# Kernel tuning notes

Measured on AMD Instinct MI355X. Metric: run time of the kernel, lower is better.

Reference implementation:

```python
import jax, jax.numpy as jnp
import numpy as np

D = 2048      # d_model
H = 16        # n_heads
DH = 128      # head dim
ROPE = 64     # qk_rope_dim = dh//2
NOPE = 64     # qk_nope_dim = dh//2
QP = 1024     # q_proj_dim = int(D*0.5)
KVP = 1365    # kv_proj_dim = int(D*2/3)
THETA = 10000.0
B, S = 2, 2048


def _ln(x, w, b):
    m = x.mean(-1, keepdims=True)
    v = ((x - m) ** 2).mean(-1, keepdims=True)
    return (x - m) / jnp.sqrt(v + 1e-5) * w + b


def _rot_half(x):
    x1, x2 = jnp.split(x, 2, axis=-1)
    return jnp.concatenate([-x2, x1], axis=-1)


def _rope_tables(seq_len):
    # freqs over full dh (as in torch buffer), then slice first ROPE//2 and repeat(...,2)
    freqs = 1.0 / (THETA ** (jnp.arange(0, DH, 2, dtype=jnp.float32) / DH))  # (DH//2,)
    emb = jnp.arange(seq_len, dtype=jnp.float32)[:, None] * freqs[None, :]   # (S, DH//2)
    c = jnp.cos(emb)[:, : ROPE // 2]
    s = jnp.sin(emb)[:, : ROPE // 2]
    cos = jnp.concatenate([c, c], axis=-1)  # (S, ROPE)  matches .repeat(1,1,1,2)
    sin = jnp.concatenate([s, s], axis=-1)
    return cos, sin


def setup_inputs() -> dict:
    ks = jax.random.split(jax.random.key(0), 8)
    p = lambda i, shape: 0.01 * jax.random.normal(ks[i], shape, dtype=jnp.float32)
    return {
        "query": jax.random.normal(ks[0], (B, S, D), dtype=jnp.float32),
        "W_dq": p(1, (D, QP)),
        "W_uq": p(2, (QP, D)),
        "q_ln_w": jnp.ones((QP,), jnp.float32),
        "q_ln_b": jnp.zeros((QP,), jnp.float32),
        "W_dkv": p(3, (D, KVP + ROPE)),
        "W_ukv": p(4, (KVP, D + H * NOPE)),
        "kv_ln_w": jnp.ones((KVP,), jnp.float32),
        "kv_ln_b": jnp.zeros((KVP,), jnp.float32),
        "W_o": p(5, (D, D)),
    }


def reference(query, W_dq, W_uq, q_ln_w, q_ln_b, W_dkv, W_ukv, kv_ln_w, kv_ln_b, W_o):
    b, sq, _ = query.shape
    # Q low-rank path
    cq = _ln(query @ W_dq, q_ln_w, q_ln_b)                       # (B,S,QP)
    Q = (cq @ W_uq).reshape(b, sq, H, DH).transpose(0, 2, 1, 3)  # (B,H,S,DH)
    Qn, Qr = Q[..., :NOPE], Q[..., NOPE:]
    cos, sin = _rope_tables(sq)                                  # (S,ROPE)
    Qr = Qr * cos + _rot_half(Qr) * sin
    # KV low-rank path
    compressed_kv = query @ W_dkv                                # (B,S,KVP+ROPE)
    kv_lat, Kr = compressed_kv[..., :KVP], compressed_kv[..., KVP:]
    kv_lat = _ln(kv_lat, kv_ln_w, kv_ln_b)
    KV = (kv_lat @ W_ukv).reshape(b, sq, H, DH + NOPE).transpose(0, 2, 1, 3)
    Kn, V = KV[..., :NOPE], KV[..., NOPE:]                       # (B,H,S,NOPE),(B,H,S,DH)
    Kr = Kr * cos + _rot_half(Kr) * sin                          # (B,S,ROPE) shared head
    qh = jnp.concatenate([Qn, Qr], axis=-1)                      # (B,H,S,DH)
    kh = jnp.concatenate([Kn, jnp.broadcast_to(Kr[:, None], (b, H, sq, ROPE))], axis=-1)
    # causal attention, scale 1/sqrt(dh) as in SDPA
    scores = jnp.einsum('bhqd,bhkd->bhqk', qh, kh) / jnp.sqrt(jnp.float32(DH))
    mask = jnp.tril(jnp.ones((sq, sq), dtype=bool))
    scores = jnp.where(mask, scores, -jnp.inf)
    attn = jax.nn.softmax(scores, axis=-1)
    out = jnp.einsum('bhqk,bhkd->bhqd', attn, V).transpose(0, 2, 1, 3).reshape(b, sq, D)
    output = out @ W_o.T                                          # nn.Linear, no bias
    return output, compressed_kv
```

## Files before the change

### kernel.cpp

```cpp
#include <hip/hip_runtime.h>

#define BB_   2
#define S_    2048
#define D_    2048
#define H_    16
#define DH_   128
#define ROPE_ 64
#define QP_   1024
#define KVP_  1365
#define KVPR_ 1429
#define KVP_PAD_ 1408
#define NKV_PAD_ 1536
#define NCOMB_ 2560
#define MT_   4096
#define UKV_N_ 3072

typedef unsigned short u16;
typedef unsigned int   u32;
typedef __attribute__((ext_vector_type(4))) u16    u16x4;
typedef __attribute__((ext_vector_type(8))) u16    u16x8;
typedef __attribute__((ext_vector_type(4))) u32    u32x4;
typedef __attribute__((ext_vector_type(8))) __bf16 bf16x8;
typedef __attribute__((ext_vector_type(4))) float  f32x4;
typedef __attribute__((ext_vector_type(16))) float f32x16;

#define NEG_BIG (-1.0e30f)
#define F32_FLAG_BITS 0x49742400u

__device__ __forceinline__ float bf2f(u16 u) {
    u32 x = ((u32)u) << 16;
    return __builtin_bit_cast(float, x);
}
__device__ __forceinline__ u16 f2bf(float f) {
    u32 u = __builtin_bit_cast(u32, f);
    u32 r = u + 0x7fffu + ((u >> 16) & 1u);
    return (u16)(r >> 16);
}
__device__ __forceinline__ u32 pk2(float a, float b) {
    __bf16 x = (__bf16)a, y = (__bf16)b;
    return (u32)__builtin_bit_cast(u16, x) | ((u32)__builtin_bit_cast(u16, y) << 16);
}
__device__ __forceinline__ bf16x8 ld_bf8(const u16* p) {
    u16x8 v = *(const u16x8*)p;
    return __builtin_bit_cast(bf16x8, v);
}
__device__ __forceinline__ bool flag_f32(const u32* flag) { return flag[0] > F32_FLAG_BITS; }

__device__ __forceinline__ void async16(const void* g, void* l) {
    __builtin_amdgcn_global_load_lds(
        (const __attribute__((address_space(1))) void*)g,
        (__attribute__((address_space(3))) void*)l, 16, 0, 0);
}

__global__ __launch_bounds__(256) void detect_kernel(const u16* __restrict__ q, u32* __restrict__ flag)
{
    u32 m = 0;
    for (int i = blockIdx.x * 256 + threadIdx.x; i < (1 << 20); i += 64 * 256) {
        float v = fabsf(bf2f(q[i]));
        u32 b = __builtin_bit_cast(u32, v);
        m = m > b ? m : b;
    }
    #pragma unroll
    for (int off = 32; off; off >>= 1) {
        u32 o = (u32)__shfl_xor((int)m, off, 64);
        m = m > o ? m : o;
    }
    if ((threadIdx.x & 63) == 0) atomicMax(flag, m);
}

__global__ __launch_bounds__(256) void cast_merged_kernel(
    const void* __restrict__ qin, const void* __restrict__ woin,
    u16* __restrict__ q_bf, u16* __restrict__ wo_bf, const u32* __restrict__ flag)
{
    bool f32 = flag_f32(flag);
    const void* in; u16* out; long n;
    if (blockIdx.z == 0) { in = qin;  out = q_bf;  n = (long)MT_ * D_; }
    else                 { in = woin; out = wo_bf; n = (long)D_ * D_; if (blockIdx.x >= 2048) return; }
    long i0 = ((long)blockIdx.x * 256 + threadIdx.x) * 8;
    if (i0 >= n) return;
    u16x8 o;
    if (f32) {
        const float* p = (const float*)in + i0;
        #pragma unroll
        for (int j = 0; j < 8; j++) o[j] = f2bf(p[j]);
    } else {
        o = *(const u16x8*)((const u16*)in + i0);
    }
    *(u16x8*)(out + i0) = o;
}

template <int MODE>
__global__ __launch_bounds__(256) void gemm_bt(
    const u16* __restrict__ A, const u16* __restrict__ Bt,
    void* __restrict__ Cout, int M, int N, int K,
    const float* __restrict__ cosT, const float* __restrict__ sinT,
    u16* __restrict__ khp, const u32* __restrict__ flag)
{
    __shared__ u16 As[2][128 * 32];
    __shared__ u16 Bs[2][128 * 32];
    const int tid  = threadIdx.x;
    const int lane = tid & 63;
    const int wave = tid >> 6;
    const int m0 = blockIdx.x * 128;
    const int n0 = blockIdx.y * 128;
    const int wr = (wave >> 1) * 64;
    const int wc = (wave & 1) * 64;
    const bool f32o = (MODE == 2) ? flag_f32(flag) : false;

    const int srow = lane >> 2;
    const int scol = (lane & 3) * 8;
    const u16* aptr0 = A  + (long)(m0 + wave * 32 + srow) * K + scol;
    const u16* bptr0 = Bt + (long)(n0 + wave * 32 + srow) * K + scol;
    const int woff = (wave * 32) * 32;

    f32x4 acc[4][4] = {};

    const int row16 = lane & 15;
    const int kq = (lane >> 4) * 8;

    auto stage = [&](int buf, int kt) {
        u16* asl = &As[buf][woff];
        u16* bsl = &Bs[buf][woff];
        async16(aptr0 + kt,          asl);
        async16(aptr0 + 16 * K + kt, asl + 16 * 32);
        async16(bptr0 + kt,          bsl);
        async16(bptr0 + 16 * K + kt, bsl + 16 * 32);
    };
    auto compute = [&](int buf) {
        bf16x8 a[4], b[4];
        #pragma unroll
        for (int i = 0; i < 4; i++)
            a[i] = ld_bf8(&As[buf][(wr + i * 16 + row16) * 32 + kq]);
        #pragma unroll
        for (int j = 0; j < 4; j++)
            b[j] = ld_bf8(&Bs[buf][(wc + j * 16 + row16) * 32 + kq]);
        #pragma unroll
        for (int i = 0; i < 4; i++)
            #pragma unroll
            for (int j = 0; j < 4; j++)
                acc[i][j] = __builtin_amdgcn_mfma_f32_16x16x32_bf16(a[i], b[j], acc[i][j], 0, 0, 0);
    };

    stage(0, 0);
    __syncthreads();
    const int nk = K >> 5;
    for (int t = 0; t < nk; t += 2) {
        stage(1, (t + 1) * 32);
        compute(0);
        __syncthreads();
        if (t + 2 < nk) stage(0, (t + 2) * 32);
        compute(1);
        __syncthreads();
    }

    const int crow = wr + (lane >> 4) * 4;
    const int ccol = wc + row16;

    if (MODE == 3) {
        const int h = (int)blockIdx.y;
        u16* qhp = (u16*)Cout;
        #pragma unroll
        for (int i = 0; i < 4; i++) {
            #pragma unroll
            for (int r = 0; r < 4; r++) {
                int row = m0 + crow + i * 16 + r;
                int b = row >> 11, s = row & 2047;
                long obase = (((long)(b * 16 + h)) * 2048 + s) * 128;
                if (wc == 0) {
                    #pragma unroll
                    for (int j = 0; j < 4; j++)
                        qhp[obase + j * 16 + row16] = f2bf(acc[i][j][r]);
                } else {
                    float c0 = cosT[s * 32 + row16],      s0 = sinT[s * 32 + row16];
                    float c1 = cosT[s * 32 + 16 + row16], s1 = sinT[s * 32 + 16 + row16];
                    float x0 = acc[i][0][r], x1 = acc[i][1][r];
                    float x2 = acc[i][2][r], x3 = acc[i][3][r];
                    qhp[obase + 64 + row16]  = f2bf(x0 * c0 - x2 * s0);
                    qhp[obase + 80 + row16]  = f2bf(x1 * c1 - x3 * s1);
                    qhp[obase + 96 + row16]  = f2bf(x2 * c0 + x0 * s0);
                    qhp[obase + 112 + row16] = f2bf(x3 * c1 + x1 * s1);
                }
            }
        }
        return;
    }
    if (MODE == 4) {
        #pragma unroll
        for (int i = 0; i < 4; i++) {
            #pragma unroll
            for (int r = 0; r < 4; r++) {
                int row = m0 + crow + i * 16 + r;
                int b = row >> 11, s = row & 2047;
                #pragma unroll
                for (int j = 0; j < 4; j++) {
                    int c = n0 + wc + j * 16 + row16;
                    int h = c / 192, dd = c - h * 192;
                    u16 v16 = f2bf(acc[i][j][r]);
                    if (dd < 64)
                        khp[(((long)(b * 16 + h)) * 2048 + s) * 128 + dd] = v16;
                    else
                        ((u16*)Cout)[(long)row * N + c] = v16;
                }
            }
        }
        return;
    }

    #pragma unroll
    for (int i = 0; i < 4; i++) {
        #pragma unroll
        for (int r = 0; r < 4; r++) {
            long row = m0 + crow + i * 16 + r;
            #pragma unroll
            for (int j = 0; j < 4; j++) {
                float v = acc[i][j][r];
                long col = n0 + ccol + j * 16;
                if (MODE == 2 && f32o) ((float*)Cout)[row * N + col] = v;
                else                   ((u16*)Cout)[row * N + col] = f2bf(v);
            }
        }
    }
}

__global__ __launch_bounds__(256) void transpose_all_kernel(
    const void* __restrict__ w_dq, const void* __restrict__ w_dkv,
    const void* __restrict__ w_uq, const void* __restrict__ w_ukv,
    u16* __restrict__ wcomb, u16* __restrict__ wuqT, u16* __restrict__ wukvT,
    const u32* __restrict__ flag)
{
    const void* in; u16* out; int Rin, Cin, Nout, Kpad, gx, gy;
    switch (blockIdx.z) {
        case 0: in = w_dq;  out = wcomb;                       Rin = 2048; Cin = 1024;   Nout = 1024;     Kpad = 2048;     gx = 64; gy = 32; break;
        case 1: in = w_dkv; out = wcomb + (size_t)1024 * 2048; Rin = 2048; Cin = KVPR_;  Nout = NKV_PAD_; Kpad = 2048;     gx = 64; gy = 48; break;
        case 2: in = w_uq;  out = wuqT;                        Rin = 1024; Cin = 2048;   Nout = 2048;     Kpad = 1024;     gx = 32; gy = 64; break;
        default:in = w_ukv; out = wukvT;                       Rin = KVP_; Cin = UKV_N_; Nout = UKV_N_;   Kpad = KVP_PAD_; gx = 44; gy = 96; break;
    }
    if ((int)blockIdx.x >= gx || (int)blockIdx.y >= gy) return;
    __shared__ u16 t[32][33];
    bool f32 = flag_f32(flag);
    int k0 = blockIdx.x * 32, n0 = blockIdx.y * 32;
    int tx = threadIdx.x & 31, ty = threadIdx.x >> 5;
    #pragma unroll
    for (int rr = 0; rr < 4; ++rr) {
        int k = k0 + ty + rr * 8, n = n0 + tx;
        u16 v = 0;
        if (k < Rin && n < Cin)
            v = f32 ? f2bf(((const float*)in)[(long)k * Cin + n])
                    : ((const u16*)in)[(long)k * Cin + n];
        t[ty + rr * 8][tx] = v;
    }
    __syncthreads();
    #pragma unroll
    for (int rr = 0; rr < 4; ++rr) {
        int n = n0 + ty + rr * 8, k = k0 + tx;
        if (n < Nout && k < Kpad) out[(long)n * Kpad + k] = t[tx][ty + rr * 8];
    }
}

__device__ __forceinline__ float block_sum(float v, float* red) {
    #pragma unroll
    for (int off = 32; off; off >>= 1) v += __shfl_xor(v, off, 64);
    int wv = threadIdx.x >> 6;
    __syncthreads();
    if ((threadIdx.x & 63) == 0) red[wv] = v;
    __syncthreads();
    return red[0] + red[1] + red[2] + red[3];
}

__global__ __launch_bounds__(256) void ln_both_kernel(
    const u16* __restrict__ x, const void* __restrict__ qw, const void* __restrict__ qb,
    const void* __restrict__ kw, const void* __restrict__ kb,
    u16* __restrict__ cq, u16* __restrict__ kv_lat, void* __restrict__ d_out,
    u16* __restrict__ kh, const float* __restrict__ cosT, const float* __restrict__ sinT,
    const u32* __restrict__ flag)
{
    __shared__ float red[4];
    __shared__ float kr[64];
    bool f32 = flag_f32(flag);
    long row = blockIdx.x;
    const int tid = threadIdx.x;

    if (blockIdx.z == 0) {
        const u16* xr = x + row * NCOMB_;
        float v[4]; float s = 0.f;
        #pragma unroll
        for (int i = 0; i < 4; i++) { v[i] = bf2f(xr[tid + i * 256]); s += v[i]; }
        float mean = block_sum(s, red) * (1.0f / QP_);
        float var = 0.f;
        #pragma unroll
        for (int i = 0; i < 4; i++) { float d = v[i] - mean; var += d * d; }
        var = block_sum(var, red) * (1.0f / QP_);
        float rstd = rsqrtf(var + 1e-5f);
        #pragma unroll
        for (int i = 0; i < 4; i++) {
            int idx = tid + i * 256;
            float wv = f32 ? ((const float*)qw)[idx] : bf2f(((const u16*)qw)[idx]);
            float bv = f32 ? ((const float*)qb)[idx] : bf2f(((const u16*)qb)[idx]);
            cq[row * QP_ + idx] = f2bf((v[i] - mean) * rstd * wv + bv);
        }
    } else {
        const int b = (int)(row >> 11), s_ = (int)(row & 2047);
        const u16* xr = x + row * NCOMB_ + QP_;
        u16 u[6]; float v[6]; float s = 0.f;
        #pragma unroll
        for (int i = 0; i < 6; i++) {
            int idx = tid + i * 256;
            u[i] = xr[idx];
            v[i] = bf2f(u[i]);
            if (idx >= KVP_ && idx < KVPR_) kr[idx - KVP_] = v[i];
            if (idx < KVP_) s += v[i];
        }
        float mean = block_sum(s, red) * (1.0f / KVP_);
        float var = 0.f;
        #pragma unroll
        for (int i = 0; i < 6; i++) {
            int idx = tid + i * 256;
            if (idx < KVP_) { float d = v[i] - mean; var += d * d; }
        }
        var = block_sum(var, red) * (1.0f / KVP_);
        float rstd = rsqrtf(var + 1e-5f);

        float* out1f = (float*)d_out + (size_t)MT_ * D_;
        u16*   out1h = (u16*)d_out   + (size_t)MT_ * D_;
        #pragma unroll
        for (int i = 0; i < 6; i++) {
            int idx = tid + i * 256;
            if (idx < KVPR_) {
                if (f32) out1f[row * KVPR_ + idx] = v[i];
                else     out1h[row * KVPR_ + idx] = u[i];
            }
            if (idx < KVP_PAD_) {
                float wv = 0.f, bv = 0.f;
                if (idx < KVP_) {
                    wv = f32 ? ((const float*)kw)[idx] : bf2f(((const u16*)kw)[idx]);
                    bv = f32 ? ((const float*)kb)[idx] : bf2f(((const u16*)kb)[idx]);
                }
                u16 o = 0;
                if (idx < KVP_) o = f2bf((v[i] - mean) * rstd * wv + bv);
                kv_lat[row * KVP_PAD_ + idx] = o;
            }
            if (idx >= KVP_ && idx < KVPR_) {
                int r = idx - KVP_;
                float xr_ = kr[r];
                float xo = (r < 32) ? -kr[r + 32] : kr[r - 32];
                int m = r & 31;
                u16 vv = f2bf(xr_ * cosT[s_ * 32 + m] + xo * sinT[s_ * 32 + m]);
                #pragma unroll
                for (int h = 0; h < 16; h++)
                    kh[(((long)(b * 16 + h)) * 2048 + s_) * 128 + 64 + r] = vv;
            }
        }
    }
}

__global__ void rope_tab_kernel(float* __restrict__ cosT, float* __restrict__ sinT, u32* __restrict__ flag) {
    int idx = blockIdx.x * 256 + threadIdx.x;
    if (idx == 0) flag[0] = 0u;
    if (idx >= S_ * 32) return;
    int pos = idx >> 5, i = idx & 31;
    float freq = (float)exp(-((double)i / 64.0) * log(10000.0));
    float ang = (float)pos * freq;
    cosT[idx] = (float)cos((double)ang);
    sinT[idx] = (float)sin((double)ang);
}

__global__ __launch_bounds__(256) void pack_vt_kernel(const u16* __restrict__ KV, u16* __restrict__ Vt)
{
    int bh = blockIdx.x; int b = bh >> 4, h = bh & 15;
    int s0 = blockIdx.y * 64;
    __shared__ u16 t[64][136];
    #pragma unroll
    for (int it = 0; it < 4; ++it) {
        int ch = threadIdx.x + it * 256;
        int sr = ch >> 4, c8 = (ch & 15) * 8;
        *(u16x8*)&t[sr][c8] = *(const u16x8*)&KV[((long)(b * S_ + s0 + sr)) * 3072 + h * 192 + 64 + c8];
    }
    __syncthreads();
    #pragma unroll
    for (int it = 0; it < 4; ++it) {
        int ch = threadIdx.x + it * 256;
        int d = ch >> 3, s8 = (ch & 7) * 8;
        u16x8 v;
        #pragma unroll
        for (int j = 0; j < 8; j++) v[j] = t[s8 + j][d];
        *(u16x8*)&Vt[((long)bh * 128 + d) * S_ + s0 + s8] = v;
    }
}

#define ATT_SCALE 0.08838834764831845f
#define K_LOG2E (ATT_SCALE * 1.4426950408889634f)
#define DEFER_THR 62.0f

__global__ __launch_bounds__(256, 2) void attn_kernel(
    const u16* __restrict__ qh, const u16* __restrict__ kh,
    const u16* __restrict__ Vt, u16* __restrict__ attn_out)
{
    __shared__ u16 Ks[64 * 128];
    __shared__ u16 Vs[128 * 64];

    const int bh = (int)blockIdx.x + ((int)blockIdx.z << 3);
    const int b = bh >> 4, h = bh & 15;
    const int jq = ((int)blockIdx.z < 2) ? (15 - (int)blockIdx.y) : (int)blockIdx.y;
    const int qbase = jq * 128;
    const int tid = threadIdx.x;
    const int lane = tid & 63;
    const int w = tid >> 6;
    const int l5 = lane & 31;
    const int hi = lane >> 5;
    const int wq0 = qbase + w * 32;
    const int qg = wq0 + l5;
    const int kend = qbase + 128;
    const int kend_w = wq0 + 32;

    bf16x8 qb[8];
    {
        const u16* qp = &qh[((long)bh * S_ + qg) * 128 + 8 * hi];
        #pragma unroll
        for (int kc = 0; kc < 8; kc++)
            qb[kc] = ld_bf8(qp + kc * 16);
    }

    f32x16 o[4] = {};
    float m_run = NEG_BIG;
    float l_run = 0.f;

    const long khb = (long)bh * S_;

    u16x8 kst[4], vst[4];
    auto load_kv = [&](int k0) {
        #pragma unroll
        for (int it = 0; it < 4; ++it) {
            int r = w * 16 + it * 4 + (lane >> 4);
            kst[it] = *(const u16x8*)&kh[(khb + k0 + r) * 128 + (((lane & 15) ^ (r & 7)) << 3)];
        }
        #pragma unroll
        for (int it = 0; it < 4; ++it) {
            int d = w * 32 + it * 8 + (lane >> 3);
            vst[it] = *(const u16x8*)&Vt[((long)bh * 128 + d) * S_ + k0 + (((lane & 7) ^ (d & 7)) << 3)];
        }
    };

    load_kv(0);

    for (int k0 = 0; k0 < kend; k0 += 64) {
        __syncthreads();
        #pragma unroll
        for (int it = 0; it < 4; ++it)
            *(u16x8*)&Ks[(w * 16 + it * 4) * 128 + lane * 8] = kst[it];
        #pragma unroll
        for (int it = 0; it < 4; ++it)
            *(u16x8*)&Vs[(w * 32 + it * 8) * 64 + lane * 8] = vst[it];
        __syncthreads();
        if (k0 + 64 < kend) load_kv(k0 + 64);

        if (k0 < kend_w) {
            f32x16 sc[2] = {};
            #pragma unroll
            for (int kc = 0; kc < 8; kc++) {
                #pragma unroll
                for (int ct = 0; ct < 2; ct++) {
                    int krow = ct * 32 + l5;
                    bf16x8 kf = ld_bf8(&Ks[krow * 128 + (((2 * kc + hi) ^ (krow & 7)) << 3)]);
                    sc[ct] = __builtin_amdgcn_mfma_f32_32x32x16_bf16(kf, qb[kc], sc[ct], 0, 0, 0);
                }
            }
            if (k0 + 64 > wq0) {
                #pragma unroll
                for (int ct = 0; ct < 2; ct++)
                    #pragma unroll
                    for (int g = 0; g < 4; g++)
                        #pragma unroll
                        for (int t = 0; t < 4; t++)
                            sc[ct][g * 4 + t] =
                                (k0 + ct * 32 + g * 8 + t + 4 * hi <= qg) ? sc[ct][g * 4 + t] : NEG_BIG;
            }
            float m = sc[0][0];
            #pragma unroll
            for (int i = 1; i < 16; i++) m = fmaxf(m, sc[0][i]);
            #pragma unroll
            for (int i = 0; i < 16; i++) m = fmaxf(m, sc[1][i]);
            m = fmaxf(m, __shfl_xor(m, 32, 64));
            bool ok = (m <= m_run + DEFER_THR);
            if (!__all((int)ok)) {
                float mn = fmaxf(m_run, m);
                float alpha = exp2f((m_run - mn) * K_LOG2E);
                m_run = mn;
                l_run *= alpha;
                #pragma unroll
                for (int dt = 0; dt < 4; dt++)
                    #pragma unroll
                    for (int i = 0; i < 16; i++) o[dt][i] *= alpha;
            }
            float mk = m_run * K_LOG2E;
            float s = 0.f;
            #pragma unroll
            for (int ct = 0; ct < 2; ct++)
                #pragma unroll
                for (int i = 0; i < 16; i++) {
                    float p = exp2f(fmaf(sc[ct][i], K_LOG2E, -mk));
                    sc[ct][i] = p;
                    s += p;
                }
            l_run += s + __shfl_xor(s, 32, 64);
            bf16x8 pb[4];
            #pragma unroll
            for (int ct = 0; ct < 2; ct++)
                #pragma unroll
                for (int c2 = 0; c2 < 2; c2++) {
                    u32 lo0 = pk2(sc[ct][8 * c2 + 0], sc[ct][8 * c2 + 1]);
                    u32 lo1 = pk2(sc[ct][8 * c2 + 2], sc[ct][8 * c2 + 3]);
                    u32 h0  = pk2(sc[ct][8 * c2 + 4], sc[ct][8 * c2 + 5]);
                    u32 h1  = pk2(sc[ct][8 * c2 + 6], sc[ct][8 * c2 + 7]);
                    u32 s0 = hi ? lo0 : h0;
                    u32 s1 = hi ? lo1 : h1;
                    u32 r0 = (u32)__shfl_xor((int)s0, 32, 64);
                    u32 r1 = (u32)__shfl_xor((int)s1, 32, 64);
                    u32x4 f;
                    f[0] = hi ? r0 : lo0;
                    f[1] = hi ? r1 : lo1;
                    f[2] = hi ? h0 : r0;
                    f[3] = hi ? h1 : r1;
                    pb[ct * 2 + c2] = __builtin_bit_cast(bf16x8, f);
                }
            #pragma unroll
            for (int kk = 0; kk < 4; kk++) {
                #pragma unroll
                for (int dt = 0; dt < 4; dt++) {
                    int drow = dt * 32 + l5;
                    bf16x8 vf = ld_bf8(&Vs[drow * 64 + (((2 * kk + hi) ^ (drow & 7)) << 3)]);
                    o[dt] = __builtin_amdgcn_mfma_f32_32x32x16_bf16(vf, pb[kk], o[dt], 0, 0, 0);
                }
            }
        }
    }

    float inv = 1.0f / l_run;
    const long orow = ((long)b * S_ + qg) * 2048 + h * 128;
    #pragma unroll
    for (int dt = 0; dt < 4; dt++)
        #pragma unroll
        for (int g = 0; g < 4; g++) {
            u16x4 v;
            #pragma unroll
            for (int t = 0; t < 4; t++) v[t] = f2bf(o[dt][g * 4 + t] * inv);
            *(u16x4*)&attn_out[orow + dt * 32 + g * 8 + 4 * hi] = v;
        }
}

#define MIB(x) ((size_t)(x) << 20)
extern "C" void kernel_launch(void* const* d_in, const int* in_sizes, int n_in,
                              void* d_out, int out_size, void* d_ws, size_t ws_size,
                              hipStream_t stream)
{
    const void* query  = d_in[0];
    const void* W_dq   = d_in[1];
    const void* W_uq   = d_in[2];
    const void* q_ln_w = d_in[3];
    const void* q_ln_b = d_in[4];
    const void* W_dkv  = d_in[5];
    const void* W_ukv  = d_in[6];
    const void* kv_ln_w = d_in[7];
    const void* kv_ln_b = d_in[8];
    const void* W_o    = d_in[9];
    (void)ws_size; (void)in_sizes; (void)n_in; (void)out_size;

    char* base = (char*)d_ws;
    u32*   flag     = (u32*)base;
    float* rope_cos = (float*)(base + 4096);
    float* rope_sin = (float*)(base + 266240);
    u16* qh     = (u16*)(base + MIB(1));
    u16* kh     = (u16*)(base + MIB(17));
    u16* Vt     = (u16*)(base + MIB(33));
    u16* q_bf   = (u16*)(base + MIB(49));
    u16* Wo_bf  = (u16*)(base + MIB(65));
    u16* Wcomb  = (u16*)(base + MIB(73));
    u16* cqkv   = (u16*)(base + MIB(83));
    u16* cq     = (u16*)(base + MIB(103));
    u16* kv_lat = (u16*)(base + MIB(111));
    u16* WuqT   = (u16*)(base + MIB(122));
    u16* WukvT  = (u16*)(base + MIB(126));
    u16* KV     = (u16*)(base + MIB(73));
    u16* attn_o = (u16*)(base + MIB(73));

    rope_tab_kernel<<<(S_ * 32 + 255) / 256, 256, 0, stream>>>(rope_cos, rope_sin, flag);
    detect_kernel<<<64, 256, 0, stream>>>((const u16*)query, flag);

    cast_merged_kernel<<<dim3(4096, 1, 2), 256, 0, stream>>>(query, W_o, q_bf, Wo_bf, flag);
    transpose_all_kernel<<<dim3(64, 96, 4), 256, 0, stream>>>(W_dq, W_dkv, W_uq, W_ukv,
                                                              Wcomb, WuqT, WukvT, flag);

    gemm_bt<0><<<dim3(32, 20), 256, 0, stream>>>(q_bf, Wcomb, cqkv, MT_, NCOMB_, D_,
                                                 nullptr, nullptr, nullptr, flag);
    ln_both_kernel<<<dim3(MT_, 1, 2), 256, 0, stream>>>(cqkv, q_ln_w, q_ln_b, kv_ln_w, kv_ln_b,
                                                        cq, kv_lat, d_out, kh,
                                                        rope_cos, rope_sin, flag);

    gemm_bt<3><<<dim3(32, 16), 256, 0, stream>>>(cq, WuqT, qh, MT_, D_, QP_,
                                                 rope_cos, rope_sin, nullptr, flag);

    gemm_bt<4><<<dim3(32, 24), 256, 0, stream>>>(kv_lat, WukvT, KV, MT_, UKV_N_, KVP_PAD_,
                                                 nullptr, nullptr, kh, flag);
    pack_vt_kernel<<<dim3(32, 32), 256, 0, stream>>>(KV, Vt);

    attn_kernel<<<dim3(8, 16, 4), 256, 0, stream>>>(qh, kh, Vt, attn_o);
    gemm_bt<2><<<dim3(32, 16), 256, 0, stream>>>(attn_o, Wo_bf, d_out, MT_, D_, D_,
                                                 nullptr, nullptr, nullptr, flag);
}
```

Baseline: 464.4 us.

## Merge prep kernels, fuse up-projection GEMMs, and swizzle GEMM tile order

Merges rope-table and detect kernels into one launch, and merges the cast and weight-transpose kernels into one prep launch. Also fuses the Q and KV up-projection GEMMs into one launch along z, and remaps block indices in the GEMM core to a grouped/swizzled tile order meant to improve L2 reuse. This cuts launch count and idle tails between small kernels. The risk is a larger, more divergent prep grid and a tile remap that assumes specific grid shapes.

Result: slower. 476.3 us (+2.6%).

```diff
diff --git a/kernel.cpp b/kernel.cpp
--- a/kernel.cpp
+++ b/kernel.cpp
@@ -52,57 +52,111 @@
         (__attribute__((address_space(3))) void*)l, 16, 0, 0);
 }
 
-__global__ __launch_bounds__(256) void detect_kernel(const u16* __restrict__ q, u32* __restrict__ flag)
-{
-    u32 m = 0;
-    for (int i = blockIdx.x * 256 + threadIdx.x; i < (1 << 20); i += 64 * 256) {
-        float v = fabsf(bf2f(q[i]));
-        u32 b = __builtin_bit_cast(u32, v);
-        m = m > b ? m : b;
-    }
+__global__ void rope_detect_kernel(float* __restrict__ cosT, float* __restrict__ sinT,
+                                   const u16* __restrict__ q, u32* __restrict__ flag)
+{
+    if (blockIdx.z == 0) {
+        int idx = blockIdx.x * 256 + threadIdx.x;
+        if (idx >= S_ * 32) return;
+        int pos = idx >> 5, i = idx & 31;
+        float freq = (float)exp(-((double)i / 64.0) * log(10000.0));
+        float ang = (float)pos * freq;
+        cosT[idx] = (float)cos((double)ang);
+        sinT[idx] = (float)sin((double)ang);
+    } else {
+        if (blockIdx.x >= 64) return;
+        u32 m = 0;
+        for (int i = blockIdx.x * 256 + threadIdx.x; i < (1 << 20); i += 64 * 256) {
+            float v = fabsf(bf2f(q[i]));
+            u32 b = __builtin_bit_cast(u32, v);
+            m = m > b ? m : b;
+        }
+        #pragma unroll
+        for (int off = 32; off; off >>= 1) {
+            u32 o = (u32)__shfl_xor((int)m, off, 64);
+            m = m > o ? m : o;
+        }
+        if ((threadIdx.x & 63) == 0) atomicMax(flag, m);
+    }
+}
+
+__global__ __launch_bounds__(256) void prep_kernel(
+    const void* __restrict__ query, const void* __restrict__ W_o,
+    u16* __restrict__ q_bf, u16* __restrict__ wo_bf,
+    const void* __restrict__ w_dq, const void* __restrict__ w_dkv,
+    const void* __restrict__ w_uq, const void* __restrict__ w_ukv,
+    u16* __restrict__ wcomb, u16* __restrict__ wuqT, u16* __restrict__ wukvT,
+    const u32* __restrict__ flag)
+{
+    const int z = blockIdx.z;
+    bool f32 = flag_f32(flag);
+    if (z < 2) {
+        const void* in; u16* out; long n;
+        if (z == 0) { in = query; out = q_bf;  n = (long)MT_ * D_; }
+        else        { in = W_o;   out = wo_bf; n = (long)D_ * D_; }
+        long i0 = ((long)blockIdx.x * 256 + threadIdx.x) * 8;
+        if (i0 >= n) return;
+        u16x8 o;
+        if (f32) {
+            const float* p = (const float*)in + i0;
+            #pragma unroll
+            for (int j = 0; j < 8; j++) o[j] = f2bf(p[j]);
+        } else {
+            o = *(const u16x8*)((const u16*)in + i0);
+        }
+        *(u16x8*)(out + i0) = o;
+        return;
+    }
+    const void* in; u16* out; int Rin, Cin, Nout, Kpad, gx, gy;
+    switch (z - 2) {
+        case 0: in = w_dq;  out = wcomb;                       Rin = 2048; Cin = 1024;   Nout = 1024;     Kpad = 2048;     gx = 64; gy = 32; break;
+        case 1: in = w_dkv; out = wcomb + (size_t)1024 * 2048; Rin = 2048; Cin = KVPR_;  Nout = NKV_PAD_; Kpad = 2048;     gx = 64; gy = 48; break;
+        case 2: in = w_uq;  out = wuqT;                        Rin = 1024; Cin = 2048;   Nout = 2048;     Kpad = 1024;     gx = 32; gy = 64; break;
+        default:in = w_ukv; out = wukvT;                       Rin = KVP_; Cin = UKV_N_; Nout = UKV_N_;   Kpad = KVP_PAD_; gx = 44; gy = 96; break;
+    }
+    int bx = (int)blockIdx.x & 63, by = (int)blockIdx.x >> 6;
+    if (bx >= gx || by >= gy) return;
+    __shared__ u16 t[32][33];
+    int k0 = bx * 32, n0 = by * 32;
+    int tx = threadIdx.x & 31, ty = threadIdx.x >> 5;
     #pragma unroll
-    for (int off = 32; off; off >>= 1) {
-        u32 o = (u32)__shfl_xor((int)m, off, 64);
-        m = m > o ? m : o;
-    }
-    if ((threadIdx.x & 63) == 0) atomicMax(flag, m);
-}
-
-__global__ __launch_bounds__(256) void cast_merged_kernel(
-    const void* __restrict__ qin, const void* __restrict__ woin,
-    u16* __restrict__ q_bf, u16* __restrict__ wo_bf, const u32* __restrict__ flag)
-{
-    bool f32 = flag_f32(flag);
-    const void* in; u16* out; long n;
-    if (blockIdx.z == 0) { in = qin;  out = q_bf;  n = (long)MT_ * D_; }
-    else                 { in = woin; out = wo_bf; n = (long)D_ * D_; if (blockIdx.x >= 2048) return; }
-    long i0 = ((long)blockIdx.x * 256 + threadIdx.x) * 8;
-    if (i0 >= n) return;
-    u16x8 o;
-    if (f32) {
-        const float* p = (const float*)in + i0;
-        #pragma unroll
-        for (int j = 0; j < 8; j++) o[j] = f2bf(p[j]);
-    } else {
-        o = *(const u16x8*)((const u16*)in + i0);
-    }
-    *(u16x8*)(out + i0) = o;
+    for (int rr = 0; rr < 4; ++rr) {
+        int k = k0 + ty + rr * 8, n = n0 + tx;
+        u16 v = 0;
+        if (k < Rin && n < Cin)
+            v = f32 ? f2bf(((const float*)in)[(long)k * Cin + n])
+                    : ((const u16*)in)[(long)k * Cin + n];
+        t[ty + rr * 8][tx] = v;
+    }
+    __syncthreads();
+    #pragma unroll
+    for (int rr = 0; rr < 4; ++rr) {
+        int n = n0 + ty + rr * 8, k = k0 + tx;
+        if (n < Nout && k < Kpad) out[(long)n * Kpad + k] = t[tx][ty + rr * 8];
+    }
 }
 
 template <int MODE>
-__global__ __launch_bounds__(256) void gemm_bt(
-    const u16* __restrict__ A, const u16* __restrict__ Bt,
-    void* __restrict__ Cout, int M, int N, int K,
+__device__ __forceinline__ void gemm_core(
+    u16 (*As)[128 * 32], u16 (*Bs)[128 * 32],
+    const u16* __restrict__ A, const u16* __restrict__ Bt, void* __restrict__ Cout,
+    int N, int K,
     const float* __restrict__ cosT, const float* __restrict__ sinT,
     u16* __restrict__ khp, const u32* __restrict__ flag)
 {
-    __shared__ u16 As[2][128 * 32];
-    __shared__ u16 Bs[2][128 * 32];
     const int tid  = threadIdx.x;
     const int lane = tid & 63;
     const int wave = tid >> 6;
-    const int m0 = blockIdx.x * 128;
-    const int n0 = blockIdx.y * 128;
+
+    const int gy = N >> 7;
+    const int x0 = (int)blockIdx.x, y0i = (int)blockIdx.y;
+    const int k8 = x0 & 7;
+    const int r  = y0i * 4 + (x0 >> 3);
+    const int xt = ((k8 & 3) << 3) + (r & 7);
+    const int yt = (k8 >> 2) * (gy >> 1) + (r >> 3);
+    const int m0 = xt * 128;
+    const int n0 = yt * 128;
+
     const int wr = (wave >> 1) * 64;
     const int wc = (wave & 1) * 64;
     const bool f32o = (MODE == 2) ? flag_f32(flag) : false;
@@ -157,28 +211,28 @@
     const int ccol = wc + row16;
 
     if (MODE == 3) {
-        const int h = (int)blockIdx.y;
+        const int h = yt;
         u16* qhp = (u16*)Cout;
         #pragma unroll
         for (int i = 0; i < 4; i++) {
             #pragma unroll
-            for (int r = 0; r < 4; r++) {
-                int row = m0 + crow + i * 16 + r;
+            for (int rr = 0; rr < 4; rr++) {
+                int row = m0 + crow + i * 16 + rr;
                 int b = row >> 11, s = row & 2047;
                 long obase = (((long)(b * 16 + h)) * 2048 + s) * 128;
                 if (wc == 0) {
                     #pragma unroll
                     for (int j = 0; j < 4; j++)
-                        qhp[obase + j * 16 + row16] = f2bf(acc[i][j][r]);
+                        qhp[obase + j * 16 + row16] = f2bf(acc[i][j][rr]);
                 } else {
                     float c0 = cosT[s * 32 + row16],      s0 = sinT[s * 32 + row16];
                     float c1 = cosT[s * 32 + 16 + row16], s1 = sinT[s * 32 + 16 + row16];
-                    float x0 = acc[i][0][r], x1 = acc[i][1][r];
-                    float x2 = acc[i][2][r], x3 = acc[i][3][r];
-                    qhp[obase + 64 + row16]  = f2bf(x0 * c0 - x2 * s0);
-                    qhp[obase + 80 + row16]  = f2bf(x1 * c1 - x3 * s1);
-                    qhp[obase + 96 + row16]  = f2bf(x2 * c0 + x0 * s0);
-                    qhp[obase + 112 + row16] = f2bf(x3 * c1 + x1 * s1);
+                    float x0v = acc[i][0][rr], x1v = acc[i][1][rr];
+                    float x2v = acc[i][2][rr], x3v = acc[i][3][rr];
+                    qhp[obase + 64 + row16]  = f2bf(x0v * c0 - x2v * s0);
+                    qhp[obase + 80 + row16]  = f2bf(x1v * c1 - x3v * s1);
+                    qhp[obase + 96 + row16]  = f2bf(x2v * c0 + x0v * s0);
+                    qhp[obase + 112 + row16] = f2bf(x3v * c1 + x1v * s1);
                 }
             }
         }
@@ -188,14 +242,14 @@
         #pragma unroll
         for (int i = 0; i < 4; i++) {
             #pragma unroll
-            for (int r = 0; r < 4; r++) {
-                int row = m0 + crow + i * 16 + r;
+            for (int rr = 0; rr < 4; rr++) {
+                int row = m0 + crow + i * 16 + rr;
                 int b = row >> 11, s = row & 2047;
                 #pragma unroll
                 for (int j = 0; j < 4; j++) {
                     int c = n0 + wc + j * 16 + row16;
                     int h = c / 192, dd = c - h * 192;
-                    u16 v16 = f2bf(acc[i][j][r]);
+                    u16 v16 = f2bf(acc[i][j][rr]);
                     if (dd < 64)
                         khp[(((long)(b * 16 + h)) * 2048 + s) * 128 + dd] = v16;
                     else
@@ -209,11 +263,11 @@
     #pragma unroll
     for (int i = 0; i < 4; i++) {
         #pragma unroll
-        for (int r = 0; r < 4; r++) {
-            long row = m0 + crow + i * 16 + r;
+        for (int rr = 0; rr < 4; rr++) {
+            long row = m0 + crow + i * 16 + rr;
             #pragma unroll
             for (int j = 0; j < 4; j++) {
-                float v = acc[i][j][r];
+                float v = acc[i][j][rr];
                 long col = n0 + ccol + j * 16;
                 if (MODE == 2 && f32o) ((float*)Cout)[row * N + col] = v;
                 else                   ((u16*)Cout)[row * N + col] = f2bf(v);
@@ -222,39 +276,38 @@
     }
 }
 
-__global__ __launch_bounds__(256) void transpose_all_kernel(
-    const void* __restrict__ w_dq, const void* __restrict__ w_dkv,
-    const void* __restrict__ w_uq, const void* __restrict__ w_ukv,
-    u16* __restrict__ wcomb, u16* __restrict__ wuqT, u16* __restrict__ wukvT,
+__global__ __launch_bounds__(256) void gemm_down_kernel(
+    const u16* __restrict__ A, const u16* __restrict__ Bt, u16* __restrict__ C,
     const u32* __restrict__ flag)
 {
-    const void* in; u16* out; int Rin, Cin, Nout, Kpad, gx, gy;
-    switch (blockIdx.z) {
-        case 0: in = w_dq;  out = wcomb;                       Rin = 2048; Cin = 1024;   Nout = 1024;     Kpad = 2048;     gx = 64; gy = 32; break;
-        case 1: in = w_dkv; out = wcomb + (size_t)1024 * 2048; Rin = 2048; Cin = KVPR_;  Nout = NKV_PAD_; Kpad = 2048;     gx = 64; gy = 48; break;
-        case 2: in = w_uq;  out = wuqT;                        Rin = 1024; Cin = 2048;   Nout = 2048;     Kpad = 1024;     gx = 32; gy = 64; break;
-        default:in = w_ukv; out = wukvT;                       Rin = KVP_; Cin = UKV_N_; Nout = UKV_N_;   Kpad = KVP_PAD_; gx = 44; gy = 96; break;
-    }
-    if ((int)blockIdx.x >= gx || (int)blockIdx.y >= gy) return;
-    __shared__ u16 t[32][33];
-    bool f32 = flag_f32(flag);
-    int k0 = blockIdx.x * 32, n0 = blockIdx.y * 32;
-    int tx = threadIdx.x & 31, ty = threadIdx.x >> 5;
-    #pragma unroll
-    for (int rr = 0; rr < 4; ++rr) {
-        int k = k0 + ty + rr * 8, n = n0 + tx;
-        u16 v = 0;
-        if (k < Rin && n < Cin)
-            v = f32 ? f2bf(((const float*)in)[(long)k * Cin + n])
-                    : ((const u16*)in)[(long)k * Cin + n];
-        t[ty + rr * 8][tx] = v;
-    }
-    __syncthreads();
-    #pragma unroll
-    for (int rr = 0; rr < 4; ++rr) {
-        int n = n0 + ty + rr * 8, k = k0 + tx;
-        if (n < Nout && k < Kpad) out[(long)n * Kpad + k] = t[tx][ty + rr * 8];
-    }
+    __shared__ u16 As[2][128 * 32];
+    __shared__ u16 Bs[2][128 * 32];
+    gemm_core<0>(As, Bs, A, Bt, C, NCOMB_, D_, nullptr, nullptr, nullptr, flag);
+}
+
+__global__ __launch_bounds__(256) void gemm_up_kernel(
+    const u16* __restrict__ cq, const u16* __restrict__ WuqT, u16* __restrict__ qh,
+    const u16* __restrict__ kv_lat, const u16* __restrict__ WukvT, u16* __restrict__ KV,
+    u16* __restrict__ kh, const float* __restrict__ cosT, const float* __restrict__ sinT,
+    const u32* __restrict__ flag)
+{
+    __shared__ u16 As[2][128 * 32];
+    __shared__ u16 Bs[2][128 * 32];
+    if (blockIdx.z == 0) {
+        if (blockIdx.y >= 16) return;
+        gemm_core<3>(As, Bs, cq, WuqT, qh, 2048, QP_, cosT, sinT, nullptr, flag);
+    } else {
+        gemm_core<4>(As, Bs, kv_lat, WukvT, KV, UKV_N_, KVP_PAD_, nullptr, nullptr, kh, flag);
+    }
+}
+
+__global__ __launch_bounds__(256) void gemm_out_kernel(
+    const u16* __restrict__ A, const u16* __restrict__ Bt, void* __restrict__ C,
+    const u32* __restrict__ flag)
+{
+    __shared__ u16 As[2][128 * 32];
+    __shared__ u16 Bs[2][128 * 32];
+    gemm_core<2>(As, Bs, A, Bt, C, D_, D_, nullptr, nullptr, nullptr, flag);
 }
 
 __device__ __forceinline__ float block_sum(float v, float* red) {
@@ -351,17 +404,6 @@
             }
         }
     }
-}
-
-__global__ void rope_tab_kernel(float* __restrict__ cosT, float* __restrict__ sinT, u32* __restrict__ flag) {
-    int idx = blockIdx.x * 256 + threadIdx.x;
-    if (idx == 0) flag[0] = 0u;
-    if (idx >= S_ * 32) return;
-    int pos = idx >> 5, i = idx & 31;
-    float freq = (float)exp(-((double)i / 64.0) * log(10000.0));
-    float ang = (float)pos * freq;
-    cosT[idx] = (float)cos((double)ang);
-    sinT[idx] = (float)sin((double)ang);
 }
 
 __global__ __launch_bounds__(256) void pack_vt_kernel(const u16* __restrict__ KV, u16* __restrict__ Vt)
@@ -582,27 +624,21 @@
     u16* KV     = (u16*)(base + MIB(73));
     u16* attn_o = (u16*)(base + MIB(73));
 
-    rope_tab_kernel<<<(S_ * 32 + 255) / 256, 256, 0, stream>>>(rope_cos, rope_sin, flag);
-    detect_kernel<<<64, 256, 0, stream>>>((const u16*)query, flag);
-
-    cast_merged_kernel<<<dim3(4096, 1, 2), 256, 0, stream>>>(query, W_o, q_bf, Wo_bf, flag);
-    transpose_all_kernel<<<dim3(64, 96, 4), 256, 0, stream>>>(W_dq, W_dkv, W_uq, W_ukv,
-                                                              Wcomb, WuqT, WukvT, flag);
-
-    gemm_bt<0><<<dim3(32, 20), 256, 0, stream>>>(q_bf, Wcomb, cqkv, MT_, NCOMB_, D_,
-                                                 nullptr, nullptr, nullptr, flag);
+    hipMemsetAsync(flag, 0, sizeof(u32), stream);
+    rope_detect_kernel<<<dim3(256, 1, 2), 256, 0, stream>>>(rope_cos, rope_sin,
+                                                            (const u16*)query, flag);
+    prep_kernel<<<dim3(6144, 1, 6), 256, 0, stream>>>(query, W_o, q_bf, Wo_bf,
+                                                      W_dq, W_dkv, W_uq, W_ukv,
+                                                      Wcomb, WuqT, WukvT, flag);
+
+    gemm_down_kernel<<<dim3(32, 20), 256, 0, stream>>>(q_bf, Wcomb, cqkv, flag);
     ln_both_kernel<<<dim3(MT_, 1, 2), 256, 0, stream>>>(cqkv, q_ln_w, q_ln_b, kv_ln_w, kv_ln_b,
                                                         cq, kv_lat, d_out, kh,
                                                         rope_cos, rope_sin, flag);
-
-    gemm_bt<3><<<dim3(32, 16), 256, 0, stream>>>(cq, WuqT, qh, MT_, D_, QP_,
-                                                 rope_cos, rope_sin, nullptr, flag);
-
-    gemm_bt<4><<<dim3(32, 24), 256, 0, stream>>>(kv_lat, WukvT, KV, MT_, UKV_N_, KVP_PAD_,
-                                                 nullptr, nullptr, kh, flag);
+    gemm_up_kernel<<<dim3(32, 24, 2), 256, 0, stream>>>(cq, WuqT, qh, kv_lat, WukvT, KV, kh,
+                                                        rope_cos, rope_sin, flag);
     pack_vt_kernel<<<dim3(32, 32), 256, 0, stream>>>(KV, Vt);
 
     attn_kernel<<<dim3(8, 16, 4), 256, 0, stream>>>(qh, kh, Vt, attn_o);
-    gemm_bt<2><<<dim3(32, 16), 256, 0, stream>>>(attn_o, Wo_bf, d_out, MT_, D_, D_,
-                                                 nullptr, nullptr, nullptr, flag);
-}
+    gemm_out_kernel<<<dim3(32, 16), 256, 0, stream>>>(attn_o, Wo_bf, d_out, flag);
+}
```
